# Optimization experiments

Measured on AMD Instinct MI355X. Metric: run time of the kernel, lower is better.

Reference implementation:

```python
import jax, jax.numpy as jnp
import numpy as np
import math

# Model config (see init_kwargs)
E = 1024   # emb_size
H = 8      # ffwd_num_head
D = 128    # ffwd_head_size (E == H*D)
NE = 16    # ffwd_num_expert
A = 2      # ffwd_num_expert_active
S = 256    # ffwd_expert_size
B = 2      # batch_size_fwd
T = 2048   # context_window
NUM_BLOCK = 12


def setup_inputs() -> dict:
    key = jax.random.key(0)
    ks = jax.random.split(key, 5)
    x = jax.random.normal(ks[0], (B, T, E), jnp.float32)
    # fc_in_fused: Linear(E, 4E+NE, bias=False), torch weight shape (out,in)
    w_in = 0.02 * jax.random.normal(ks[1], (4 * E + NE, E), jnp.float32)
    # fc_out_fused: Linear(2E, E), std 0.02/sqrt(num_block)
    w_out = (0.02 / math.sqrt(NUM_BLOCK)) * jax.random.normal(ks[2], (E, 2 * E), jnp.float32)
    # k_ffwd/v_ffwd: original (1,H,NE*S,D); stored here as (NE,H,S,D) for per-expert scan
    k_ffwd = 0.02 * jax.random.normal(ks[3], (NE, H, S, D), jnp.float32)
    v_ffwd = 0.02 * jax.random.normal(ks[4], (NE, H, S, D), jnp.float32)
    return {"x": x, "w_in": w_in, "w_out": w_out, "k_ffwd": k_ffwd, "v_ffwd": v_ffwd}


def _rope(t):
    # Standard half-split RoPE, base 10000. t: (B,T,H,D)
    half = t.shape[-1] // 2
    inv_freq = 1.0 / (10000.0 ** (jnp.arange(half, dtype=jnp.float32) / half))
    ang = jnp.arange(t.shape[1], dtype=jnp.float32)[:, None] * inv_freq  # (T, half)
    cos = jnp.cos(ang)[None, :, None, :]
    sin = jnp.sin(ang)[None, :, None, :]
    t1, t2 = t[..., :half], t[..., half:]
    return jnp.concatenate([t1 * cos - t2 * sin, t1 * sin + t2 * cos], axis=-1)


def reference(x, w_in, w_out, k_ffwd, v_ffwd):
    Bx, Tx, _ = x.shape
    h = x @ w_in.T  # (B,T,4E+NE)
    q_f, q_a, k_a, v_a, router_logits = jnp.split(h, [E, 2 * E, 3 * E, 4 * E], axis=-1)

    # top-k routing (order of the k slots is irrelevant: outputs are summed)
    gate_logits, assign = jax.lax.top_k(router_logits, A)  # (B,T,A)
    gate = jax.nn.sigmoid(gate_logits)

    # --- attention half: causal softmax attention, scale 1/sqrt(D), with RoPE ---
    q = _rope(q_a.reshape(Bx, Tx, H, D))
    k = _rope(k_a.reshape(Bx, Tx, H, D))
    v = v_a.reshape(Bx, Tx, H, D)
    scores = jnp.einsum('bqhd,bkhd->bhqk', q, k) / math.sqrt(D)
    causal = jnp.tril(jnp.ones((Tx, Tx), dtype=bool))
    scores = jnp.where(causal, scores, -jnp.inf)
    p = jax.nn.softmax(scores, axis=-1)
    attn_out = jnp.einsum('bhqk,bkhd->bqhd', p, v).reshape(Bx, Tx, E)

    # --- MoE-FFN half, expressed as attention with score_mod log1p(gelu):
    # exp(lse)*softmax recovers sum_s (1+gelu(q.k_s)) v_s; subtracting sum_s v_s
    # leaves sum_s gelu(q.k_s) v_s over the assigned expert's slots. ---
    qf = q_f.reshape(Bx, Tx, H, D)

    def step(acc, ekv):
        e, ke, ve = ekv  # ke, ve: (H,S,D)
        s = jnp.einsum('bthd,hsd->bths', qf, ke)
        a = jax.nn.gelu(s, approximate=False)  # torch F.gelu default = exact erf
        o = jnp.einsum('bths,hsd->bthd', a, ve)
        g = jnp.sum(jnp.where(assign == e, gate, 0.0), axis=-1)  # (B,T)
        return acc + g[..., None, None] * o, None

    acc0 = jnp.zeros((Bx, Tx, H, D), x.dtype)
    ffwd_out, _ = jax.lax.scan(step, acc0, (jnp.arange(NE), k_ffwd, v_ffwd))
    ffwd_out = ffwd_out.reshape(Bx, Tx, E)

    out = jnp.concatenate([attn_out, ffwd_out], axis=-1) @ w_out.T  # (B,T,E)
    return out
```

## Files before the change

kernel.cpp:

```cpp
#include <hip/hip_runtime.h>
#include <hip/hip_bf16.h>
#include <math.h>

#define E 1024
#define NHP 4096
#define NEXP 16
#define HH 8
#define DD 128
#define SS 256
#define BB 2
#define TT 2048
#define BT 4096

typedef __attribute__((ext_vector_type(8))) short bf16x8;
typedef __attribute__((ext_vector_type(4))) float f32x4;

#define GLDS16(g, s) __builtin_amdgcn_global_load_lds( \
    (const __attribute__((address_space(1))) void*)(g), \
    (__attribute__((address_space(3))) void*)(s), 16, 0, 0)

__device__ __forceinline__ ushort f2b(float f) {
    union { float f; unsigned u; } v; v.f = f;
    unsigned r = (v.u + 0x7FFFu + ((v.u >> 16) & 1u)) >> 16;
    return (ushort)r;
}
__device__ __forceinline__ float b2f(ushort u) {
    union { unsigned u; float f; } v; v.u = ((unsigned)u) << 16;
    return v.f;
}
__device__ __forceinline__ float gelu_fast(float x) {
    float u2 = x * x;
    float tu = x * (1.5957691216f + 0.0713548163f * u2);
    float e = __expf(tu);
    float sig = 1.f - __builtin_amdgcn_rcpf(e + 1.f);
    return x * sig;
}

__global__ void cvtk(const float4* __restrict__ in, ushort4* __restrict__ outp, int n4)
{
    int i = blockIdx.x * blockDim.x + threadIdx.x;
    if (i >= n4) return;
    float4 f = in[i];
    ushort4 u;
    u.x = f2b(f.x); u.y = f2b(f.y); u.z = f2b(f.z); u.w = f2b(f.w);
    outp[i] = u;
}

template<int BF16OUT>
__global__ __launch_bounds__(256) void gemm_bf16(
    const ushort* __restrict__ A, int lda,
    const ushort* __restrict__ B, int ldb,
    void* __restrict__ Cv, int ldc, int K)
{
    __shared__ ushort As[128 * 32];
    __shared__ ushort Bs[128 * 32];
    const int t = threadIdx.x;
    const int l = t & 63, w = t >> 6;
    const int m0 = blockIdx.y * 128, n0 = blockIdx.x * 128;
    const int wr = w >> 1, wc = w & 1;
    const int fr = l & 15, fg = l >> 4;

    const ushort* Ag = A + (size_t)(m0 + w * 16 + (l >> 2)) * lda + (l & 3) * 8;
    const ushort* Bg = B + (size_t)(n0 + w * 16 + (l >> 2)) * ldb + (l & 3) * 8;
    ushort* AsW = As + (w * 16) * 32;
    ushort* BsW = Bs + (w * 16) * 32;

    f32x4 acc[4][4];
    #pragma unroll
    for (int i = 0; i < 4; ++i)
        #pragma unroll
        for (int j = 0; j < 4; ++j) { acc[i][j][0]=0.f; acc[i][j][1]=0.f; acc[i][j][2]=0.f; acc[i][j][3]=0.f; }

    for (int k0 = 0; k0 < K; k0 += 32) {
        GLDS16(Ag + k0, AsW);
        GLDS16(Ag + (size_t)64 * lda + k0, AsW + 64 * 32);
        GLDS16(Bg + k0, BsW);
        GLDS16(Bg + (size_t)64 * ldb + k0, BsW + 64 * 32);
        __syncthreads();
        bf16x8 a[4], b[4];
        #pragma unroll
        for (int mi = 0; mi < 4; ++mi)
            a[mi] = *(const bf16x8*)(As + (wr * 64 + mi * 16 + fr) * 32 + fg * 8);
        #pragma unroll
        for (int ni = 0; ni < 4; ++ni)
            b[ni] = *(const bf16x8*)(Bs + (wc * 64 + ni * 16 + fr) * 32 + fg * 8);
        #pragma unroll
        for (int mi = 0; mi < 4; ++mi)
            #pragma unroll
            for (int ni = 0; ni < 4; ++ni)
                acc[mi][ni] = __builtin_amdgcn_mfma_f32_16x16x32_bf16(a[mi], b[ni], acc[mi][ni], 0, 0, 0);
        __syncthreads();
    }
    #pragma unroll
    for (int mi = 0; mi < 4; ++mi)
        #pragma unroll
        for (int ni = 0; ni < 4; ++ni) {
            const int row = m0 + wr * 64 + mi * 16 + fg * 4;
            const int col = n0 + wc * 64 + ni * 16 + fr;
            #pragma unroll
            for (int r = 0; r < 4; ++r) {
                if (BF16OUT)
                    ((ushort*)Cv)[(size_t)(row + r) * ldc + col] = f2b(acc[mi][ni][r]);
                else
                    ((float*)Cv)[(size_t)(row + r) * ldc + col] = acc[mi][ni][r];
            }
        }
}

__global__ __launch_bounds__(256) void router_logits(
    const float* __restrict__ x, const float* __restrict__ w_in,
    float* __restrict__ gval, int* __restrict__ eidx)
{
    const int m = blockIdx.x * 4 + (threadIdx.x >> 6);
    const int lane = threadIdx.x & 63;

    const float* xp = x + (size_t)m * 1024 + lane * 4;
    float4 xv0 = *(const float4*)(xp);
    float4 xv1 = *(const float4*)(xp + 256);
    float4 xv2 = *(const float4*)(xp + 512);
    float4 xv3 = *(const float4*)(xp + 768);

    float p[16];
    #pragma unroll
    for (int e = 0; e < 16; ++e) {
        const float* wp = w_in + (size_t)(4096 + e) * 1024 + lane * 4;
        float4 w0 = *(const float4*)(wp);
        float4 w1 = *(const float4*)(wp + 256);
        float4 w2 = *(const float4*)(wp + 512);
        float4 w3 = *(const float4*)(wp + 768);
        float s0 = xv0.x * w0.x + xv0.y * w0.y + xv0.z * w0.z + xv0.w * w0.w;
        float s1 = xv1.x * w1.x + xv1.y * w1.y + xv1.z * w1.z + xv1.w * w1.w;
        float s2 = xv2.x * w2.x + xv2.y * w2.y + xv2.z * w2.z + xv2.w * w2.w;
        float s3 = xv3.x * w3.x + xv3.y * w3.y + xv3.z * w3.z + xv3.w * w3.w;
        p[e] = (s0 + s1) + (s2 + s3);
    }
    #pragma unroll
    for (int d = 1; d < 64; d <<= 1) {
        #pragma unroll
        for (int e = 0; e < 16; ++e)
            p[e] += __shfl_xor(p[e], d);
    }
    float best = -1e30f; int bi = 0;
    #pragma unroll
    for (int e = 0; e < 16; ++e)
        if (p[e] > best) { best = p[e]; bi = e; }
    float best2 = -1e30f; int bi2 = 0;
    #pragma unroll
    for (int e = 0; e < 16; ++e)
        if (e != bi && p[e] > best2) { best2 = p[e]; bi2 = e; }

    if (lane == 0) {
        gval[m * 2 + 0] = 1.f / (1.f + __expf(-best));
        gval[m * 2 + 1] = 1.f / (1.f + __expf(-best2));
        eidx[m * 2 + 0] = bi;
        eidx[m * 2 + 1] = bi2;
    }
}

__global__ __launch_bounds__(256) void build_lists(
    const int* __restrict__ eidx,
    int* __restrict__ counts, int* __restrict__ plist)
{
    const int e = blockIdx.x;
    const int t = threadIdx.x;
    const int w = t >> 6, lane = t & 63;
    __shared__ int wbase[4];
    __shared__ int running;
    if (t == 0) running = 0;
    __syncthreads();
    for (int c = 0; c < 2 * BT; c += 256) {
        const int p = c + t;
        const bool match = (eidx[p] == e);
        unsigned long long mask = __ballot(match);
        int lpre = __popcll(mask & ((lane == 63) ? 0x7FFFFFFFFFFFFFFFull
                                                 : ((1ull << lane) - 1ull)));
        if (lane == 0) wbase[w] = __popcll(mask);
        __syncthreads();
        int pre = running;
        #pragma unroll
        for (int i = 0; i < 4; ++i) if (i < w) pre += wbase[i];
        const int tot = wbase[0] + wbase[1] + wbase[2] + wbase[3];
        if (match) plist[e * BT + pre + lpre] = p;
        __syncthreads();
        if (t == 0) running += tot;
        __syncthreads();
    }
    if (t == 0) counts[e] = running;
}

__global__ void rope2(const ushort* __restrict__ hb,
                      ushort* __restrict__ qb, ushort* __restrict__ kb)
{
    int m = blockIdx.x;
    int t = threadIdx.x;
    int hd = t >> 6, j = t & 63;
    int tok = m & 2047, b = m >> 11;
    float invf = __expf(-(float)j * (9.210340371976184f / 64.f));
    float ang = (float)tok * invf;
    float s, c;
    sincosf(ang, &s, &c);
    const ushort* base = hb + (size_t)m * NHP + E + hd * DD;
    float q1 = b2f(base[j]), q2 = b2f(base[j + 64]);
    float k1 = b2f(base[E + j]), k2 = b2f(base[E + j + 64]);
    float qa = q1 * c - q2 * s, qbv = q1 * s + q2 * c;
    float ka = k1 * c - k2 * s, kbv = k1 * s + k2 * c;
    size_t rowb = ((size_t)(b * 8 + hd) * 2048 + tok) * 256;
    int sw = (tok & 7) << 4;
    *(ushort*)((char*)qb + rowb + ((2 * j) ^ sw))        = f2b(qa);
    *(ushort*)((char*)qb + rowb + ((2 * (j + 64)) ^ sw)) = f2b(qbv);
    *(ushort*)((char*)kb + rowb + ((2 * j) ^ sw))        = f2b(ka);
    *(ushort*)((char*)kb + rowb + ((2 * (j + 64)) ^ sw)) = f2b(kbv);
}

__global__ __launch_bounds__(256) void vtrans(const ushort* __restrict__ hb,
                                              ushort* __restrict__ vtb)
{
    __shared__ ushort T[64][132];
    int bh = blockIdx.y, ck = blockIdx.x;
    int b = bh >> 3, hd = bh & 7;
    int t = threadIdx.x;
    int tok0 = ck * 64;
    #pragma unroll
    for (int it = 0; it < 8; ++it) {
        int idx = it * 256 + t, r = idx >> 5, c4 = idx & 31;
        ushort4 f = *(const ushort4*)(hb + (size_t)(b * 2048 + tok0 + r) * NHP + 3 * E + hd * DD + c4 * 4);
        T[r][c4 * 4 + 0] = f.x; T[r][c4 * 4 + 1] = f.y;
        T[r][c4 * 4 + 2] = f.z; T[r][c4 * 4 + 3] = f.w;
    }
    __syncthreads();
    int g = t >> 4, fr = t & 15;
    #pragma unroll
    for (int dd = 0; dd < 8; ++dd) {
        int d = g + dd * 16;
        ushort4 u;
        u.x = T[4 * fr + 0][d]; u.y = T[4 * fr + 1][d];
        u.z = T[4 * fr + 2][d]; u.w = T[4 * fr + 3][d];
        size_t ob = ((size_t)(bh * 128 + d) * 2048 + tok0) * 2;
        *(ushort4*)((char*)vtb + ob + ((8 * fr) ^ ((d & 7) << 4))) = u;
    }
}

__global__ __launch_bounds__(256) void cvt_kv(
    const float* __restrict__ kf, const float* __restrict__ vf,
    ushort* __restrict__ kfb, ushort* __restrict__ vtf)
{
    __shared__ float T[64][132];
    int eh = blockIdx.y, st = blockIdx.x;
    int s0 = st * 64;
    int t = threadIdx.x;
    const float* kbp = kf + (size_t)eh * SS * DD + (size_t)s0 * DD;
    const float* vbp = vf + (size_t)eh * SS * DD + (size_t)s0 * DD;
    for (int i = t; i < 64 * 32; i += 256) {
        int r = i >> 5, c4 = i & 31;
        float4 f = *(const float4*)(kbp + (size_t)r * DD + c4 * 4);
        ushort4 u;
        u.x = f2b(f.x); u.y = f2b(f.y); u.z = f2b(f.z); u.w = f2b(f.w);
        *(ushort4*)((char*)kfb + ((size_t)eh * 256 + s0 + r) * 256 + ((c4 * 8) ^ ((r & 7) << 4))) = u;
    }
    for (int i = t; i < 64 * 32; i += 256) {
        int r = i >> 5, c4 = i & 31;
        float4 f = *(const float4*)(vbp + (size_t)r * DD + c4 * 4);
        T[r][c4 * 4 + 0] = f.x; T[r][c4 * 4 + 1] = f.y;
        T[r][c4 * 4 + 2] = f.z; T[r][c4 * 4 + 3] = f.w;
    }
    __syncthreads();
    int g = t >> 4, fr = t & 15;
    #pragma unroll
    for (int dd = 0; dd < 8; ++dd) {
        int d = g + dd * 16;
        ushort4 u;
        u.x = f2b(T[4 * fr + 0][d]); u.y = f2b(T[4 * fr + 1][d]);
        u.z = f2b(T[4 * fr + 2][d]); u.w = f2b(T[4 * fr + 3][d]);
        size_t ob = ((size_t)eh * 128 + d) * 512 + s0 * 2;
        *(ushort4*)((char*)vtf + ob + ((8 * fr) ^ ((d & 7) << 4))) = u;
    }
}

__global__ __launch_bounds__(512, 1) void attn_mfma(
    const ushort* __restrict__ qb, const ushort* __restrict__ kb,
    const ushort* __restrict__ vtb, ushort* __restrict__ catb)
{
    __shared__ ushort Ks[2][128 * 128];
    __shared__ ushort Vs[2][128 * 128];
    __shared__ ushort Ps[8][16 * 72];
    __shared__ float  LlS[8][16];

    const int t = threadIdx.x, l = t & 63, w = t >> 6;
    const int fr = l & 15, fg = l >> 4;
    const int wl = w & 3, hh = w >> 2;
    const int lin = blockIdx.x;
    const int bh = (lin & 7) * 2 + (lin >> 7);
    const int tpair = (lin >> 3) & 15;
    const int swz = (fr & 7) << 4;
    ushort* Pw = (ushort*)Ps[w];

    #pragma unroll 1
    for (int pass = 0; pass < 2; ++pass) {
        const int qt = pass ? (31 - tpair) : tpair;
        const int qbase = qt * 64;
        const int nkt = (qt + 2) >> 1;
        const int qg = qbase + wl * 16 + fg * 4;

        bf16x8 qreg[4];
        {
            const char* qrow = (const char*)qb + ((size_t)(bh * 2048 + qbase + wl * 16 + fr)) * 256;
            #pragma unroll
            for (int ks = 0; ks < 4; ++ks)
                qreg[ks] = *(const bf16x8*)(qrow + ((ks * 64 + fg * 16) ^ swz));
        }
        {
            const char* ksrc = (const char*)kb + ((size_t)(bh * 2048 + w * 16)) * 256;
            const char* vsrc = (const char*)vtb + ((size_t)(bh * 128 + w * 16)) * 4096;
            #pragma unroll
            for (int i = 0; i < 4; ++i) {
                GLDS16(ksrc + (size_t)(i * 4 + (l >> 4)) * 256 + (l & 15) * 16,
                       (char*)Ks[0] + (w * 16 + i * 4) * 256);
                GLDS16(vsrc + (size_t)(i * 4 + (l >> 4)) * 4096 + (l & 15) * 16,
                       (char*)Vs[0] + (w * 16 + i * 4) * 256);
            }
        }

        f32x4 po[8];
        #pragma unroll
        for (int i = 0; i < 8; ++i) { po[i][0]=0.f; po[i][1]=0.f; po[i][2]=0.f; po[i][3]=0.f; }
        float lrow[4] = {0.f, 0.f, 0.f, 0.f};

        asm volatile("s_waitcnt vmcnt(0)" ::: "memory");
        __syncthreads();

        for (int kt = 0; kt < nkt; ++kt) {
            const int cur = kt & 1;
            if (kt + 1 < nkt) {
                const int kvn = (kt + 1) * 128;
                const char* ksrc = (const char*)kb + ((size_t)(bh * 2048 + kvn + w * 16)) * 256;
                const char* vsrc = (const char*)vtb + ((size_t)(bh * 128 + w * 16)) * 4096 + kvn * 2;
                #pragma unroll
                for (int i = 0; i < 4; ++i) {
                    GLDS16(ksrc + (size_t)(i * 4 + (l >> 4)) * 256 + (l & 15) * 16,
                           (char*)Ks[cur ^ 1] + (w * 16 + i * 4) * 256);
                    GLDS16(vsrc + (size_t)(i * 4 + (l >> 4)) * 4096 + (l & 15) * 16,
                           (char*)Vs[cur ^ 1] + (w * 16 + i * 4) * 256);
                }
            }
            const int kvb = kt * 128;

            f32x4 s[4];
            #pragma unroll
            for (int i = 0; i < 4; ++i) { s[i][0]=0.f; s[i][1]=0.f; s[i][2]=0.f; s[i][3]=0.f; }
            __builtin_amdgcn_s_setprio(1);
            #pragma unroll
            for (int ks = 0; ks < 4; ++ks) {
                #pragma unroll
                for (int fn = 0; fn < 4; ++fn) {
                    const int brow = hh * 64 + fn * 16 + fr;
                    bf16x8 bb = *(const bf16x8*)((const char*)Ks[cur] + brow * 256 + ((ks * 64 + fg * 16) ^ swz));
                    s[fn] = __builtin_amdgcn_mfma_f32_16x16x32_bf16(qreg[ks], bb, s[fn], 0, 0, 0);
                }
            }
            __builtin_amdgcn_s_setprio(0);

            const int colbase = kvb + hh * 64;
            const bool needmask = (colbase + 64 > qbase + wl * 16);
            float ps[4] = {0.f, 0.f, 0.f, 0.f};
            #pragma unroll
            for (int fn = 0; fn < 4; ++fn)
                #pragma unroll
                for (int r = 0; r < 4; ++r) {
                    float v = s[fn][r] * 0.08838834764831845f;
                    bool masked = needmask && (colbase + fn * 16 + fr > qg + r);
                    float p = masked ? 0.f : __expf(v);
                    ps[r] += p;
                    Pw[(fg * 4 + r) * 72 + fn * 16 + fr] = f2b(p);
                }
            #pragma unroll
            for (int r = 0; r < 4; ++r) {
                float s2 = ps[r];
                s2 += __shfl_xor(s2, 1);
                s2 += __shfl_xor(s2, 2);
                s2 += __shfl_xor(s2, 4);
                s2 += __shfl_xor(s2, 8);
                lrow[r] += s2;
            }

            asm volatile("s_waitcnt lgkmcnt(0)" ::: "memory");
            __builtin_amdgcn_sched_barrier(0);

            __builtin_amdgcn_s_setprio(1);
            #pragma unroll
            for (int ks2 = 0; ks2 < 2; ++ks2) {
                bf16x8 pa = *(const bf16x8*)((const char*)Pw + fr * 144 + ks2 * 64 + fg * 16);
                #pragma unroll
                for (int fn2 = 0; fn2 < 8; ++fn2) {
                    const int vrow = fn2 * 16 + fr;
                    bf16x8 bv = *(const bf16x8*)((const char*)Vs[cur] + vrow * 256 + ((hh * 128 + ks2 * 64 + fg * 16) ^ swz));
                    po[fn2] = __builtin_amdgcn_mfma_f32_16x16x32_bf16(pa, bv, po[fn2], 0, 0, 0);
                }
            }
            __builtin_amdgcn_s_setprio(0);

            asm volatile("s_waitcnt vmcnt(0)" ::: "memory");
            __syncthreads();
        }

        if (fr == 0) {
            #pragma unroll
            for (int r = 0; r < 4; ++r)
                LlS[w][fg * 4 + r] = lrow[r];
        }
        __syncthreads();
        float linv[4];
        #pragma unroll
        for (int r = 0; r < 4; ++r)
            linv[r] = 1.f / (lrow[r] + LlS[w ^ 4][fg * 4 + r]);
        float* PO = (float*)&Ks[0][0];
        if (hh == 1) {
            #pragma unroll
            for (int fn2 = 0; fn2 < 8; ++fn2)
                #pragma unroll
                for (int r = 0; r < 4; ++r)
                    PO[(wl * 16 + fg * 4 + r) * 128 + fn2 * 16 + fr] = po[fn2][r];
        }
        __syncthreads();
        if (hh == 0) {
            const int mg = (bh >> 3) * 2048 + qbase + wl * 16 + fg * 4;
            #pragma unroll
            for (int r = 0; r < 4; ++r) {
                #pragma unroll
                for (int fn2 = 0; fn2 < 8; ++fn2) {
                    float v = po[fn2][r] + PO[(wl * 16 + fg * 4 + r) * 128 + fn2 * 16 + fr];
                    catb[(size_t)(mg + r) * 2048 + (bh & 7) * 128 + fn2 * 16 + fr] = f2b(v * linv[r]);
                }
            }
        }
        __syncthreads();
    }
}

__global__ __launch_bounds__(256, 1) void ffn_mfma2(
    const ushort* __restrict__ hb,
    const float* __restrict__ gv,
    const int* __restrict__ counts,
    const int* __restrict__ plist,
    const ushort* __restrict__ kfb, const ushort* __restrict__ vtf,
    ushort* __restrict__ pairout)
{
    __shared__ ushort Ks[256 * 128];
    __shared__ ushort Vs[128 * 256];
    __shared__ ushort Qs[64 * 128];
    __shared__ ushort Ps[4][16 * 72];

    const int t = threadIdx.x, l = t & 63, w = t >> 6;
    const int fr = l & 15, fg = l >> 4;
    const int half = blockIdx.x, hd = blockIdx.y, e = blockIdx.z;
    const int eh = e * HH + hd;
    const int n_e = counts[e];

    {
        const char* kbase = (const char*)kfb + (size_t)eh * 65536;
        const char* vbase = (const char*)vtf + (size_t)eh * 65536;
        #pragma unroll
        for (int i = 0; i < 16; ++i) {
            GLDS16(kbase + (w * 64 + i * 4) * 256 + l * 16, (char*)Ks + (w * 64 + i * 4) * 256);
            GLDS16(vbase + w * 16384 + i * 1024 + l * 16, (char*)Vs + w * 16384 + i * 1024);
        }
    }
    __syncthreads();

    const int arow = w * 16 + fr;
    const int aswz = (arow & 7) << 4;
    ushort* Pw = (ushort*)Ps[w];
    const int rl4 = l >> 4;
    const int lb = (l & 15) * 16;

    for (int tb = half * 64; tb < n_e; tb += 128) {
        #pragma unroll
        for (int i = 0; i < 4; ++i) {
            int row = w * 16 + i * 4 + rl4;
            int gr = tb + row;
            int p = plist[e * BT + min(gr, n_e - 1)];
            int m = p >> 1;
            const char* src = (const char*)hb + (size_t)m * 8192 + hd * 256 + (lb ^ ((row & 7) << 4));
            GLDS16(src, (char*)Qs + (w * 16 + i * 4) * 256);
        }
        asm volatile("s_waitcnt vmcnt(0)" ::: "memory");

        f32x4 po[8];
        #pragma unroll
        for (int i = 0; i < 8; ++i) { po[i][0]=0.f; po[i][1]=0.f; po[i][2]=0.f; po[i][3]=0.f; }

        #pragma unroll
        for (int kt = 0; kt < 4; ++kt) {
            const int kvb = kt * 64;
            f32x4 s[4];
            #pragma unroll
            for (int i = 0; i < 4; ++i) { s[i][0]=0.f; s[i][1]=0.f; s[i][2]=0.f; s[i][3]=0.f; }
            #pragma unroll
            for (int ks = 0; ks < 4; ++ks) {
                bf16x8 a = *(const bf16x8*)((const char*)Qs + arow * 256 + ((ks * 64 + fg * 16) ^ aswz));
                #pragma unroll
                for (int fn = 0; fn < 4; ++fn) {
                    const int brow = kvb + fn * 16 + fr;
                    bf16x8 bb = *(const bf16x8*)((const char*)Ks + brow * 256 + ((ks * 64 + fg * 16) ^ ((brow & 7) << 4)));
                    s[fn] = __builtin_amdgcn_mfma_f32_16x16x32_bf16(a, bb, s[fn], 0, 0, 0);
                }
            }
            #pragma unroll
            for (int fn = 0; fn < 4; ++fn)
                #pragma unroll
                for (int r = 0; r < 4; ++r)
                    Pw[(fg * 4 + r) * 72 + fn * 16 + fr] = f2b(gelu_fast(s[fn][r]));
            asm volatile("s_waitcnt lgkmcnt(0)" ::: "memory");
            #pragma unroll
            for (int ks2 = 0; ks2 < 2; ++ks2) {
                bf16x8 pa = *(const bf16x8*)((const char*)Pw + fr * 144 + ks2 * 64 + fg * 16);
                #pragma unroll
                for (int fn2 = 0; fn2 < 8; ++fn2) {
                    const int vrow = fn2 * 16 + fr;
                    bf16x8 bv = *(const bf16x8*)((const char*)Vs + vrow * 512 + kt * 128 + ((ks2 * 64 + fg * 16) ^ ((vrow & 7) << 4)));
                    po[fn2] = __builtin_amdgcn_mfma_f32_16x16x32_bf16(pa, bv, po[fn2], 0, 0, 0);
                }
            }
        }
        const int rloc = w * 16 + fg * 4;
        #pragma unroll
        for (int r = 0; r < 4; ++r) {
            int gr = tb + rloc + r;
            if (gr < n_e) {
                int p = plist[e * BT + gr];
                float g = gv[p];
                #pragma unroll
                for (int fn2 = 0; fn2 < 8; ++fn2)
                    pairout[(size_t)p * 1024 + hd * DD + fn2 * 16 + fr] = f2b(g * po[fn2][r]);
            }
        }
    }
}

__global__ void combine_kernel(const ushort* __restrict__ po, ushort* __restrict__ catb)
{
    int i = blockIdx.x * blockDim.x + threadIdx.x;
    if (i >= BT * 128) return;
    int m = i >> 7, c = i & 127;
    const ushort* a = po + (size_t)(2 * m) * 1024 + c * 8;
    const ushort* b = po + (size_t)(2 * m + 1) * 1024 + c * 8;
    ushort4 a0 = *(const ushort4*)a, a1 = *(const ushort4*)(a + 4);
    ushort4 b0 = *(const ushort4*)b, b1 = *(const ushort4*)(b + 4);
    ushort4 o0, o1;
    o0.x = f2b(b2f(a0.x) + b2f(b0.x)); o0.y = f2b(b2f(a0.y) + b2f(b0.y));
    o0.z = f2b(b2f(a0.z) + b2f(b0.z)); o0.w = f2b(b2f(a0.w) + b2f(b0.w));
    o1.x = f2b(b2f(a1.x) + b2f(b1.x)); o1.y = f2b(b2f(a1.y) + b2f(b1.y));
    o1.z = f2b(b2f(a1.z) + b2f(b1.z)); o1.w = f2b(b2f(a1.w) + b2f(b1.w));
    ushort* dst = catb + (size_t)m * 2048 + 1024 + c * 8;
    *(ushort4*)dst = o0;
    *(ushort4*)(dst + 4) = o1;
}

extern "C" void kernel_launch(void* const* d_in, const int* in_sizes, int n_in,
                              void* d_out, int out_size, void* d_ws, size_t ws_size,
                              hipStream_t stream)
{
    const float* x     = (const float*)d_in[0];
    const float* w_in  = (const float*)d_in[1];
    const float* w_out = (const float*)d_in[2];
    const float* kf    = (const float*)d_in[3];
    const float* vf    = (const float*)d_in[4];
    float* out = (float*)d_out;

    char* W = (char*)d_ws;
    ushort* hb      = (ushort*)(W + 0);
    ushort* xb      = (ushort*)(W + 33554432);
    ushort* wib     = (ushort*)(W + 41943040);
    ushort* kfb     = xb;
    ushort* vtf     = wib;
    ushort* wob     = (ushort*)(W + 50331648);
    ushort* qb2     = (ushort*)(W + 54525952);
    ushort* kb2     = (ushort*)(W + 62914560);
    ushort* vtb     = (ushort*)(W + 71303168);
    ushort* catb    = (ushort*)(W + 79691776);
    ushort* pairout = (ushort*)(W + 96468992);
    float*  gv      = (float*)(W + 113246208);
    int*    counts  = (int*)(W + 113278976);
    int*    plist   = (int*)(W + 113279040);
    int*    eidx    = (int*)(W + 113541184);

    cvtk<<<4096, 256, 0, stream>>>((const float4*)x, (ushort4*)xb, 4096 * 1024 / 4);
    cvtk<<<4096, 256, 0, stream>>>((const float4*)w_in, (ushort4*)wib, 4096 * 1024 / 4);
    cvtk<<<2048, 256, 0, stream>>>((const float4*)w_out, (ushort4*)wob, 1024 * 2048 / 4);

    router_logits<<<BT / 4, 256, 0, stream>>>(x, w_in, gv, eidx);
    build_lists<<<NEXP, 256, 0, stream>>>(eidx, counts, plist);

    gemm_bf16<1><<<dim3(32, 32), 256, 0, stream>>>(xb, 1024, wib, 1024, hb, NHP, 1024);

    rope2<<<BT, 512, 0, stream>>>(hb, qb2, kb2);
    vtrans<<<dim3(32, 16), 256, 0, stream>>>(hb, vtb);
    cvt_kv<<<dim3(4, NEXP * HH), 256, 0, stream>>>(kf, vf, kfb, vtf);

    attn_mfma<<<dim3(256), 512, 0, stream>>>(qb2, kb2, vtb, catb);

    ffn_mfma2<<<dim3(2, HH, NEXP), 256, 0, stream>>>(hb, gv, counts, plist, kfb, vtf, pairout);
    combine_kernel<<<2048, 256, 0, stream>>>(pairout, catb);

    gemm_bf16<0><<<dim3(8, 32), 256, 0, stream>>>(catb, 2048, wob, 2048, out, 1024, 2048);
}
```

Baseline: 259.7 us.

## Swizzle GEMM operand layouts in global memory and double the GEMM k-tile

The bf16 conversion kernels, the attention writer and the combine kernel now store GEMM operands with an XOR swizzle of 16-byte chunks keyed on the row. The GEMM loads 64-wide k slices straight into LDS and reads them back with the same swizzle, which avoids LDS bank conflicts, and it runs two MFMA sub-steps per barrier pair. This halves the number of synchronisation rounds and makes LDS reads conflict-free, at the cost of coupling every producer kernel to the swizzled layout. The ffn path reads hb, which is not swizzled and is unaffected.

Result: faster. 243.6 us (-6.2%).

```diff
diff --git a/kernel.cpp b/kernel.cpp
--- a/kernel.cpp
+++ b/kernel.cpp
@@ -36,14 +36,21 @@
     return x * sig;
 }
 
-__global__ void cvtk(const float4* __restrict__ in, ushort4* __restrict__ outp, int n4)
-{
-    int i = blockIdx.x * blockDim.x + threadIdx.x;
-    if (i >= n4) return;
-    float4 f = in[i];
-    ushort4 u;
-    u.x = f2b(f.x); u.y = f2b(f.y); u.z = f2b(f.z); u.w = f2b(f.w);
-    outp[i] = u;
+__global__ void cvtk_swz(const float* __restrict__ in, ushort* __restrict__ outp,
+                         int kshift, int n)
+{
+    int i = (blockIdx.x * blockDim.x + threadIdx.x) * 8;
+    if (i >= n) return;
+    int row = i >> kshift;
+    int colb = (i - (row << kshift)) * 2;
+    float4 f0 = *(const float4*)(in + i);
+    float4 f1 = *(const float4*)(in + i + 4);
+    ushort4 u0, u1;
+    u0.x = f2b(f0.x); u0.y = f2b(f0.y); u0.z = f2b(f0.z); u0.w = f2b(f0.w);
+    u1.x = f2b(f1.x); u1.y = f2b(f1.y); u1.z = f2b(f1.z); u1.w = f2b(f1.w);
+    char* dst = (char*)outp + ((size_t)row << (kshift + 1)) + (colb ^ ((row & 7) << 4));
+    *(ushort4*)dst = u0;
+    *(ushort4*)(dst + 8) = u1;
 }
 
 template<int BF16OUT>
@@ -52,18 +59,19 @@
     const ushort* __restrict__ B, int ldb,
     void* __restrict__ Cv, int ldc, int K)
 {
-    __shared__ ushort As[128 * 32];
-    __shared__ ushort Bs[128 * 32];
+    __shared__ ushort As[128 * 64];
+    __shared__ ushort Bs[128 * 64];
     const int t = threadIdx.x;
     const int l = t & 63, w = t >> 6;
     const int m0 = blockIdx.y * 128, n0 = blockIdx.x * 128;
     const int wr = w >> 1, wc = w & 1;
     const int fr = l & 15, fg = l >> 4;
 
-    const ushort* Ag = A + (size_t)(m0 + w * 16 + (l >> 2)) * lda + (l & 3) * 8;
-    const ushort* Bg = B + (size_t)(n0 + w * 16 + (l >> 2)) * ldb + (l & 3) * 8;
-    ushort* AsW = As + (w * 16) * 32;
-    ushort* BsW = Bs + (w * 16) * 32;
+    const int srow = w * 32 + (l >> 3);
+    const int sboff = (l & 7) * 16;
+    const char* Ag = (const char*)A + ((size_t)(m0 + srow) * lda) * 2 + sboff;
+    const char* Bg = (const char*)B + ((size_t)(n0 + srow) * ldb) * 2 + sboff;
+    const int aswz = (fr & 7) << 4;
 
     f32x4 acc[4][4];
     #pragma unroll
@@ -71,24 +79,28 @@
         #pragma unroll
         for (int j = 0; j < 4; ++j) { acc[i][j][0]=0.f; acc[i][j][1]=0.f; acc[i][j][2]=0.f; acc[i][j][3]=0.f; }
 
-    for (int k0 = 0; k0 < K; k0 += 32) {
-        GLDS16(Ag + k0, AsW);
-        GLDS16(Ag + (size_t)64 * lda + k0, AsW + 64 * 32);
-        GLDS16(Bg + k0, BsW);
-        GLDS16(Bg + (size_t)64 * ldb + k0, BsW + 64 * 32);
-        __syncthreads();
-        bf16x8 a[4], b[4];
-        #pragma unroll
-        for (int mi = 0; mi < 4; ++mi)
-            a[mi] = *(const bf16x8*)(As + (wr * 64 + mi * 16 + fr) * 32 + fg * 8);
-        #pragma unroll
-        for (int ni = 0; ni < 4; ++ni)
-            b[ni] = *(const bf16x8*)(Bs + (wc * 64 + ni * 16 + fr) * 32 + fg * 8);
-        #pragma unroll
-        for (int mi = 0; mi < 4; ++mi)
+    for (int k0b = 0; k0b < K * 2; k0b += 128) {
+        #pragma unroll
+        for (int i = 0; i < 4; ++i) {
+            GLDS16(Ag + (size_t)(i * 8) * lda * 2 + k0b, (char*)As + (w * 32 + i * 8) * 128);
+            GLDS16(Bg + (size_t)(i * 8) * ldb * 2 + k0b, (char*)Bs + (w * 32 + i * 8) * 128);
+        }
+        __syncthreads();
+        #pragma unroll
+        for (int ksub = 0; ksub < 2; ++ksub) {
+            bf16x8 a[4], b[4];
+            #pragma unroll
+            for (int mi = 0; mi < 4; ++mi)
+                a[mi] = *(const bf16x8*)((const char*)As + (wr * 64 + mi * 16 + fr) * 128 + ((ksub * 64 + fg * 16) ^ aswz));
             #pragma unroll
             for (int ni = 0; ni < 4; ++ni)
-                acc[mi][ni] = __builtin_amdgcn_mfma_f32_16x16x32_bf16(a[mi], b[ni], acc[mi][ni], 0, 0, 0);
+                b[ni] = *(const bf16x8*)((const char*)Bs + (wc * 64 + ni * 16 + fr) * 128 + ((ksub * 64 + fg * 16) ^ aswz));
+            #pragma unroll
+            for (int mi = 0; mi < 4; ++mi)
+                #pragma unroll
+                for (int ni = 0; ni < 4; ++ni)
+                    acc[mi][ni] = __builtin_amdgcn_mfma_f32_16x16x32_bf16(a[mi], b[ni], acc[mi][ni], 0, 0, 0);
+        }
         __syncthreads();
     }
     #pragma unroll
@@ -425,10 +437,12 @@
             const int mg = (bh >> 3) * 2048 + qbase + wl * 16 + fg * 4;
             #pragma unroll
             for (int r = 0; r < 4; ++r) {
+                const int rswz = ((mg + r) & 7) << 4;
                 #pragma unroll
                 for (int fn2 = 0; fn2 < 8; ++fn2) {
                     float v = po[fn2][r] + PO[(wl * 16 + fg * 4 + r) * 128 + fn2 * 16 + fr];
-                    catb[(size_t)(mg + r) * 2048 + (bh & 7) * 128 + fn2 * 16 + fr] = f2b(v * linv[r]);
+                    int colb = ((bh & 7) * 128 + fn2 * 16 + fr) * 2;
+                    *(ushort*)((char*)catb + (size_t)(mg + r) * 4096 + (colb ^ rswz)) = f2b(v * linv[r]);
                 }
             }
         }
@@ -550,9 +564,9 @@
     o0.z = f2b(b2f(a0.z) + b2f(b0.z)); o0.w = f2b(b2f(a0.w) + b2f(b0.w));
     o1.x = f2b(b2f(a1.x) + b2f(b1.x)); o1.y = f2b(b2f(a1.y) + b2f(b1.y));
     o1.z = f2b(b2f(a1.z) + b2f(b1.z)); o1.w = f2b(b2f(a1.w) + b2f(b1.w));
-    ushort* dst = catb + (size_t)m * 2048 + 1024 + c * 8;
+    char* dst = (char*)catb + (size_t)m * 4096 + 2048 + ((c * 16) ^ ((m & 7) << 4));
     *(ushort4*)dst = o0;
-    *(ushort4*)(dst + 4) = o1;
+    *(ushort4*)(dst + 8) = o1;
 }
 
 extern "C" void kernel_launch(void* const* d_in, const int* in_sizes, int n_in,
@@ -583,9 +597,9 @@
     int*    plist   = (int*)(W + 113279040);
     int*    eidx    = (int*)(W + 113541184);
 
-    cvtk<<<4096, 256, 0, stream>>>((const float4*)x, (ushort4*)xb, 4096 * 1024 / 4);
-    cvtk<<<4096, 256, 0, stream>>>((const float4*)w_in, (ushort4*)wib, 4096 * 1024 / 4);
-    cvtk<<<2048, 256, 0, stream>>>((const float4*)w_out, (ushort4*)wob, 1024 * 2048 / 4);
+    cvtk_swz<<<2048, 256, 0, stream>>>(x, xb, 10, 4096 * 1024);
+    cvtk_swz<<<2048, 256, 0, stream>>>(w_in, wib, 10, 4096 * 1024);
+    cvtk_swz<<<1024, 256, 0, stream>>>(w_out, wob, 11, 1024 * 2048);
 
     router_logits<<<BT / 4, 256, 0, stream>>>(x, w_in, gv, eidx);
     build_lists<<<NEXP, 256, 0, stream>>>(eidx, counts, plist);
```
